# Performance work log

Measured on AMD Instinct MI355X. Metric: run time of the kernel, lower is better.

The kernel has to match this reference:

```python
import jax, jax.numpy as jnp
from jax import lax
import numpy as np

D_MODEL = 1024
D_STATE = 128
D_CONV = 4
EXPAND = 2
HEADDIM = 64
CHUNK = 10
D_INNER = EXPAND * D_MODEL          # 2048
NHEADS = D_INNER // HEADDIM         # 32
CONV_DIM = D_INNER + 2 * D_STATE    # 2304
BATCH, SEQ = 2, 1000


def setup_inputs() -> dict:
    key = jax.random.key(0)
    ks = jax.random.split(key, 9)
    n = lambda k, shp, sc: jax.random.normal(k, shp, dtype=jnp.float32) * sc
    return {
        "x": n(ks[0], (BATCH, SEQ, D_MODEL), 1.0),
        "W_in": n(ks[1], (2 * D_INNER + 2 * D_STATE + NHEADS, D_MODEL), 0.02),
        "conv_w": n(ks[2], (CONV_DIM, D_CONV), 0.2),
        "conv_b": n(ks[3], (CONV_DIM,), 0.02),
        "dt_bias": n(ks[4], (NHEADS,), 0.5),
        "A_log": jnp.log(jnp.linspace(1.0, 16.0, NHEADS)).astype(jnp.float32),
        "D": n(ks[6], (NHEADS,), 1.0),
        "norm_w": jnp.ones((D_INNER,), jnp.float32),
        "W_out": n(ks[8], (D_MODEL, D_INNER), 0.02),
    }


def segsum(x):
    # x: (..., T) -> (..., T, T) with out[i,j] = sum_{k=j+1..i} x_k for i>=j else -inf
    cs = jnp.cumsum(x, axis=-1)
    seg = cs[..., :, None] - cs[..., None, :]
    T = x.shape[-1]
    mask = jnp.tril(jnp.ones((T, T), bool))
    return jnp.where(mask, seg, -jnp.inf)


def ssd(x, A, Bm, Cm, chunk):
    # x: (b,l,h,p)  A: (b,l,h)  Bm,Cm: (b,l,n)  (ngroups=1, group dim squeezed)
    b, l, h, p = x.shape
    n = Bm.shape[-1]
    c = l // chunk
    xr = x.reshape(b, c, chunk, h, p)
    Ar = A.reshape(b, c, chunk, h).transpose(0, 3, 1, 2)      # (b,h,c,s)
    Br = Bm.reshape(b, c, chunk, n)
    Cr = Cm.reshape(b, c, chunk, n)
    Acs = jnp.cumsum(Ar, axis=-1)                              # (b,h,c,s)
    L = jnp.exp(segsum(Ar))                                    # (b,h,c,s,s)
    # intra-chunk (diagonal blocks)
    Y_diag = jnp.einsum('bcln,bcsn,bhcls,bcshp->bclhp', Cr, Br, L, xr)
    # per-chunk end states
    decay_states = jnp.exp(Acs[..., -1:] - Acs)                # (b,h,c,s)
    states = jnp.einsum('bcln,bhcl,bclhp->bchpn', Br, decay_states, xr)
    states = jnp.concatenate([jnp.zeros((b, 1, h, p, n), x.dtype), states], axis=1)
    # inter-chunk recurrence (parallel form)
    chunk_sums = jnp.pad(Acs[..., -1], ((0, 0), (0, 0), (1, 0)))  # (b,h,c+1)
    decay_chunk = jnp.exp(segsum(chunk_sums))                    # (b,h,c+1,c+1)
    new_states = jnp.einsum('bhzc,bchpn->bzhpn', decay_chunk, states)
    prev_states = new_states[:, :-1]                             # (b,c,h,p,n)
    # state -> output contribution
    Y_off = jnp.einsum('bcln,bchpn,bhcl->bclhp', Cr, prev_states, jnp.exp(Acs))
    return (Y_diag + Y_off).reshape(b, l, h, p)


def reference(x, W_in, conv_w, conv_b, dt_bias, A_log, D, norm_w, W_out):
    b, l, _ = x.shape
    zxbcdt = x @ W_in.T                                          # (b,l,4384)
    z = zxbcdt[..., :D_INNER]
    xBC = zxbcdt[..., D_INNER:D_INNER + CONV_DIM]
    dt = zxbcdt[..., D_INNER + CONV_DIM:]
    dt = jax.nn.softplus(dt + dt_bias)                           # (b,l,h)
    # causal depthwise conv1d
    xc = jnp.pad(xBC, ((0, 0), (D_CONV - 1, 0), (0, 0)))
    conv = lax.conv_general_dilated(
        xc.transpose(0, 2, 1), conv_w[:, None, :], (1,), 'VALID',
        feature_group_count=CONV_DIM,
        dimension_numbers=('NCH', 'OIH', 'NCH'))
    xBC = jax.nn.silu(conv.transpose(0, 2, 1) + conv_b)          # (b,l,conv_dim)
    x_ssm = xBC[..., :D_INNER].reshape(b, l, NHEADS, HEADDIM)
    Bm = xBC[..., D_INNER:D_INNER + D_STATE]
    Cm = xBC[..., D_INNER + D_STATE:]
    A = -jnp.exp(A_log)                                          # (h,)
    y = ssd(x_ssm * dt[..., None], A * dt, Bm, Cm, CHUNK)
    y = y + x_ssm * D[None, None, :, None]
    y = y.reshape(b, l, D_INNER)
    # gated RMSNorm
    y = y * jax.nn.silu(z)
    y = y * lax.rsqrt(jnp.mean(y * y, axis=-1, keepdims=True) + 1e-5) * norm_w
    return y @ W_out.T
```

## Files before the change

kernel.cpp:

```cpp
#include <hip/hip_runtime.h>
#include <hip/hip_bf16.h>

#define BATCHN 2
#define SEQL 1000
#define DMODEL 1024
#define DSTATE 128
#define HEADDIM 64
#define DINNER 2048
#define NHEADS 32
#define CONVDIM 2304
#define NPROJ 4384
#define TOKENS 2000
#define MPAD 2048
#define NPAD1 4480
#define QC 64
#define NCH 16

typedef __bf16 bfx8 __attribute__((ext_vector_type(8)));
typedef float fx4 __attribute__((ext_vector_type(4)));
typedef unsigned short u16x8 __attribute__((ext_vector_type(8)));

__device__ __forceinline__ unsigned short f2bf(float f) {
    unsigned int u = __builtin_bit_cast(unsigned int, f);
    u += 0x7FFFu + ((u >> 16) & 1u);
    return (unsigned short)(u >> 16);
}
__device__ __forceinline__ float bf2f(unsigned short u) {
    return __builtin_bit_cast(float, ((unsigned int)u) << 16);
}

__device__ __forceinline__ void gload16(const void* g, void* l) {
    __builtin_amdgcn_global_load_lds(
        (const __attribute__((address_space(1))) void*)g,
        (__attribute__((address_space(3))) void*)l, 16, 0, 0);
}

__global__ __launch_bounds__(256) void k_f2bf_pad(const float* __restrict__ src,
                                                  unsigned short* __restrict__ dst,
                                                  int n4src, int n4dst) {
    int i = blockIdx.x * 256 + threadIdx.x;
    if (i >= n4dst) return;
    ushort4 o = {0, 0, 0, 0};
    if (i < n4src) {
        float4 v = ((const float4*)src)[i];
        o.x = f2bf(v.x); o.y = f2bf(v.y); o.z = f2bf(v.z); o.w = f2bf(v.w);
    }
    ((ushort4*)dst)[i] = o;
}

__global__ __launch_bounds__(256) void k_dt(const float* __restrict__ x,
                                            const float* __restrict__ win,
                                            const float* __restrict__ dt_bias,
                                            float* __restrict__ dtv) {
    __shared__ float sx[8][1024];
    int t = threadIdx.x;
    int tok0 = blockIdx.x * 8;
    for (int i = t; i < 8 * 256; i += 256) {
        int tok = i >> 8, k4 = i & 255;
        ((float4*)&sx[tok][0])[k4] = ((const float4*)(x + (size_t)(tok0 + tok) * DMODEL))[k4];
    }
    __syncthreads();
    int tl = t >> 5, h = t & 31;
    const float4* wr_ = (const float4*)(win + (size_t)(2 * DINNER + 2 * DSTATE + h) * DMODEL);
    const float4* xr = (const float4*)&sx[tl][0];
    float acc = 0.f;
    #pragma unroll 4
    for (int k = 0; k < 256; ++k) {
        float4 a = xr[k], b = wr_[k];
        acc += a.x * b.x + a.y * b.y + a.z * b.z + a.w * b.w;
    }
    float v = acc + dt_bias[h];
    dtv[(size_t)(tok0 + tl) * NHEADS + h] = fmaxf(v, 0.f) + log1pf(expf(-fabsf(v)));
}

__global__ __launch_bounds__(256) void k_gemmd(const unsigned short* __restrict__ A,
                                               const unsigned short* __restrict__ B,
                                               float* __restrict__ C,
                                               int Mstore, int N, int K,
                                               int kc, size_t pstride) {
    __shared__ __attribute__((aligned(16))) unsigned short As[2][4096];
    __shared__ __attribute__((aligned(16))) unsigned short Bs[2][4096];
    int t = threadIdx.x;
    int lane = t & 63, wave = t >> 6;
    int wr = wave >> 1, wc = wave & 1;
    int m0 = blockIdx.y * 128, n0 = blockIdx.x * 128;
    int k0 = blockIdx.z * kc;
    int swcol = (((t & 3) ^ ((t >> 3) & 3)) * 8);
    const unsigned short* Ag = A + (size_t)(m0 + (t >> 2)) * K + k0 + swcol;
    const unsigned short* Bg = B + (size_t)(n0 + (t >> 2)) * K + k0 + swcol;
    int fr = lane & 15, ks = lane >> 4;
    int sl = (ks ^ ((fr >> 1) & 3)) << 3;
    fx4 acc[4][4] = {};
    gload16(Ag, &As[0][t * 8]);
    gload16(Ag + (size_t)64 * K, &As[0][2048 + t * 8]);
    gload16(Bg, &Bs[0][t * 8]);
    gload16(Bg + (size_t)64 * K, &Bs[0][2048 + t * 8]);
    __syncthreads();
    int cur = 0;
    for (int kk = 32; kk < kc; kk += 32) {
        gload16(Ag + kk, &As[cur ^ 1][t * 8]);
        gload16(Ag + (size_t)64 * K + kk, &As[cur ^ 1][2048 + t * 8]);
        gload16(Bg + kk, &Bs[cur ^ 1][t * 8]);
        gload16(Bg + (size_t)64 * K + kk, &Bs[cur ^ 1][2048 + t * 8]);
        bfx8 a[4], b[4];
        #pragma unroll
        for (int m = 0; m < 4; ++m)
            a[m] = *(const bfx8*)&As[cur][(wr * 64 + m * 16 + fr) * 32 + sl];
        #pragma unroll
        for (int n = 0; n < 4; ++n)
            b[n] = *(const bfx8*)&Bs[cur][(wc * 64 + n * 16 + fr) * 32 + sl];
        #pragma unroll
        for (int m = 0; m < 4; ++m)
            #pragma unroll
            for (int n = 0; n < 4; ++n)
                acc[m][n] = __builtin_amdgcn_mfma_f32_16x16x32_bf16(a[m], b[n], acc[m][n], 0, 0, 0);
        __syncthreads();
        cur ^= 1;
    }
    {
        bfx8 a[4], b[4];
        #pragma unroll
        for (int m = 0; m < 4; ++m)
            a[m] = *(const bfx8*)&As[cur][(wr * 64 + m * 16 + fr) * 32 + sl];
        #pragma unroll
        for (int n = 0; n < 4; ++n)
            b[n] = *(const bfx8*)&Bs[cur][(wc * 64 + n * 16 + fr) * 32 + sl];
        #pragma unroll
        for (int m = 0; m < 4; ++m)
            #pragma unroll
            for (int n = 0; n < 4; ++n)
                acc[m][n] = __builtin_amdgcn_mfma_f32_16x16x32_bf16(a[m], b[n], acc[m][n], 0, 0, 0);
    }
    float* Cz = C + (size_t)blockIdx.z * pstride;
    #pragma unroll
    for (int m = 0; m < 4; ++m) {
        int rbase = m0 + wr * 64 + m * 16 + (lane >> 4) * 4;
        #pragma unroll
        for (int i = 0; i < 4; ++i) {
            int r = rbase + i;
            if (r < Mstore) {
                #pragma unroll
                for (int n = 0; n < 4; ++n) {
                    int c = n0 + wc * 64 + n * 16 + fr;
                    if (c < N) Cz[(size_t)r * N + c] = acc[m][n][i];
                }
            }
        }
    }
}

__global__ __launch_bounds__(256) void k_red(const float* __restrict__ part,
                                             float* __restrict__ out, int n4, size_t pstride4) {
    int i = blockIdx.x * 256 + threadIdx.x;
    if (i >= n4) return;
    const float4* p = (const float4*)part;
    float4 v0 = p[i];
    float4 v1 = p[i + pstride4];
    float4 v2 = p[i + 2 * pstride4];
    float4 v3 = p[i + 3 * pstride4];
    float4 o;
    o.x = (v0.x + v1.x) + (v2.x + v3.x);
    o.y = (v0.y + v1.y) + (v2.y + v3.y);
    o.z = (v0.z + v1.z) + (v2.z + v3.z);
    o.w = (v0.w + v1.w) + (v2.w + v3.w);
    ((float4*)out)[i] = o;
}

__global__ __launch_bounds__(256) void k_conv4(const float* __restrict__ zx,
                                               const float* __restrict__ cw,
                                               const float* __restrict__ cb,
                                               float* __restrict__ xbc) {
    int idx = blockIdx.x * 256 + threadIdx.x;
    if (idx >= (TOKENS / 4) * CONVDIM) return;
    int tg = idx / CONVDIM;
    int col = idx - tg * CONVDIM;
    int b = tg / 250;
    int l0 = (tg - b * 250) * 4;
    float in[7];
    #pragma unroll
    for (int j = 0; j < 7; ++j) {
        int lj = l0 - 3 + j;
        in[j] = (lj >= 0) ? zx[(size_t)(b * SEQL + lj) * NPROJ + DINNER + col] : 0.f;
    }
    float w0 = cw[col * 4], w1 = cw[col * 4 + 1], w2 = cw[col * 4 + 2], w3 = cw[col * 4 + 3];
    float bb = cb[col];
    #pragma unroll
    for (int i = 0; i < 4; ++i) {
        float a = bb + w0 * in[i] + w1 * in[i + 1] + w2 * in[i + 2] + w3 * in[i + 3];
        xbc[(size_t)(b * SEQL + l0 + i) * CONVDIM + col] = a / (1.f + expf(-a));
    }
}

#define SCW 136
#define SWW 72
__global__ __launch_bounds__(256) void k_tile(const float* __restrict__ xbc,
                                              const float* __restrict__ dtv,
                                              const float* __restrict__ A_log,
                                              const float* __restrict__ Dp,
                                              float* __restrict__ ybuf,
                                              float* __restrict__ Sg,
                                              float* __restrict__ cumA) {
    __shared__ unsigned short sC[64 * SCW];
    __shared__ unsigned short sB[64 * SCW];
    __shared__ unsigned short sBdT[128 * SWW];
    __shared__ unsigned short sXdT[64 * SWW];
    __shared__ unsigned short sXr[64 * SWW];
    __shared__ float sAcs[64];
    __shared__ float sdt[64];
    int bid = blockIdx.x;
    int b = bid / (NHEADS * NCH);
    int r = bid % (NHEADS * NCH);
    int h = r / NCH, c = r % NCH;
    int t = threadIdx.x;
    int lane = t & 63, wave = t >> 6;
    if (t < 64) {
        int tok = c * QC + t;
        float d = (tok < SEQL) ? dtv[(size_t)(b * SEQL + tok) * NHEADS + h] : 0.f;
        float A = -expf(A_log[h]);
        float v = A * d;
        #pragma unroll
        for (int off = 1; off < 64; off <<= 1) {
            float u = __shfl_up(v, off, 64);
            if (lane >= off) v += u;
        }
        sdt[t] = d;
        sAcs[t] = v;
        cumA[(size_t)bid * 64 + t] = v;
    }
    __syncthreads();
    float Aend = sAcs[63];
    for (int i = t; i < 64 * 32; i += 256) {
        int l = i >> 5, n4 = (i & 31) * 4;
        int tok = c * QC + l;
        float4 cv = {0, 0, 0, 0}, bv = {0, 0, 0, 0};
        if (tok < SEQL) {
            const float* base = xbc + (size_t)(b * SEQL + tok) * CONVDIM;
            bv = *(const float4*)(base + DINNER + n4);
            cv = *(const float4*)(base + DINNER + DSTATE + n4);
        }
        float dec = expf(Aend - sAcs[l]);
        sC[l * SCW + n4 + 0] = f2bf(cv.x); sC[l * SCW + n4 + 1] = f2bf(cv.y);
        sC[l * SCW + n4 + 2] = f2bf(cv.z); sC[l * SCW + n4 + 3] = f2bf(cv.w);
        sB[l * SCW + n4 + 0] = f2bf(bv.x); sB[l * SCW + n4 + 1] = f2bf(bv.y);
        sB[l * SCW + n4 + 2] = f2bf(bv.z); sB[l * SCW + n4 + 3] = f2bf(bv.w);
        sBdT[(n4 + 0) * SWW + l] = f2bf(bv.x * dec);
        sBdT[(n4 + 1) * SWW + l] = f2bf(bv.y * dec);
        sBdT[(n4 + 2) * SWW + l] = f2bf(bv.z * dec);
        sBdT[(n4 + 3) * SWW + l] = f2bf(bv.w * dec);
    }
    for (int i = t; i < 64 * 16; i += 256) {
        int l = i >> 4, p4 = (i & 15) * 4;
        int tok = c * QC + l;
        float4 xv = {0, 0, 0, 0};
        if (tok < SEQL) xv = *(const float4*)(xbc + (size_t)(b * SEQL + tok) * CONVDIM + h * 64 + p4);
        float d = sdt[l];
        sXr[l * SWW + p4 + 0] = f2bf(xv.x); sXr[l * SWW + p4 + 1] = f2bf(xv.y);
        sXr[l * SWW + p4 + 2] = f2bf(xv.z); sXr[l * SWW + p4 + 3] = f2bf(xv.w);
        sXdT[(p4 + 0) * SWW + l] = f2bf(xv.x * d);
        sXdT[(p4 + 1) * SWW + l] = f2bf(xv.y * d);
        sXdT[(p4 + 2) * SWW + l] = f2bf(xv.z * d);
        sXdT[(p4 + 3) * SWW + l] = f2bf(xv.w * d);
    }
    __syncthreads();
    int fr = lane & 15, fk8 = (lane >> 4) * 8;
    int wr = wave >> 1, wc = wave & 1;
    fx4 g[2][2] = {};
    #pragma unroll
    for (int k = 0; k < 4; ++k) {
        bfx8 a0 = *(const bfx8*)&sC[(wr * 32 + fr) * SCW + k * 32 + fk8];
        bfx8 a1 = *(const bfx8*)&sC[(wr * 32 + 16 + fr) * SCW + k * 32 + fk8];
        bfx8 b0 = *(const bfx8*)&sB[(wc * 32 + fr) * SCW + k * 32 + fk8];
        bfx8 b1 = *(const bfx8*)&sB[(wc * 32 + 16 + fr) * SCW + k * 32 + fk8];
        g[0][0] = __builtin_amdgcn_mfma_f32_16x16x32_bf16(a0, b0, g[0][0], 0, 0, 0);
        g[0][1] = __builtin_amdgcn_mfma_f32_16x16x32_bf16(a0, b1, g[0][1], 0, 0, 0);
        g[1][0] = __builtin_amdgcn_mfma_f32_16x16x32_bf16(a1, b0, g[1][0], 0, 0, 0);
        g[1][1] = __builtin_amdgcn_mfma_f32_16x16x32_bf16(a1, b1, g[1][1], 0, 0, 0);
    }
    __syncthreads();
    int rb = wr * 32 + (lane >> 4) * 4;
    int cb = wc * 32 + fr;
    #pragma unroll
    for (int m = 0; m < 2; ++m)
        #pragma unroll
        for (int n = 0; n < 2; ++n)
            #pragma unroll
            for (int i = 0; i < 4; ++i) {
                int row = rb + m * 16 + i, col = cb + n * 16;
                float wv = (col <= row) ? g[m][n][i] * expf(sAcs[row] - sAcs[col]) : 0.f;
                sB[row * SWW + col] = f2bf(wv);
            }
    __syncthreads();
    fx4 yd[2][2] = {};
    fx4 sc[2][4] = {};
    #pragma unroll
    for (int k = 0; k < 2; ++k) {
        bfx8 aW0 = *(const bfx8*)&sB[(wr * 32 + fr) * SWW + k * 32 + fk8];
        bfx8 aW1 = *(const bfx8*)&sB[(wr * 32 + 16 + fr) * SWW + k * 32 + fk8];
        bfx8 bX0 = *(const bfx8*)&sXdT[(wc * 32 + fr) * SWW + k * 32 + fk8];
        bfx8 bX1 = *(const bfx8*)&sXdT[(wc * 32 + 16 + fr) * SWW + k * 32 + fk8];
        yd[0][0] = __builtin_amdgcn_mfma_f32_16x16x32_bf16(aW0, bX0, yd[0][0], 0, 0, 0);
        yd[0][1] = __builtin_amdgcn_mfma_f32_16x16x32_bf16(aW0, bX1, yd[0][1], 0, 0, 0);
        yd[1][0] = __builtin_amdgcn_mfma_f32_16x16x32_bf16(aW1, bX0, yd[1][0], 0, 0, 0);
        yd[1][1] = __builtin_amdgcn_mfma_f32_16x16x32_bf16(aW1, bX1, yd[1][1], 0, 0, 0);
        bfx8 aX0 = *(const bfx8*)&sXdT[(wr * 32 + fr) * SWW + k * 32 + fk8];
        bfx8 aX1 = *(const bfx8*)&sXdT[(wr * 32 + 16 + fr) * SWW + k * 32 + fk8];
        #pragma unroll
        for (int j = 0; j < 4; ++j) {
            bfx8 bB = *(const bfx8*)&sBdT[(wc * 64 + j * 16 + fr) * SWW + k * 32 + fk8];
            sc[0][j] = __builtin_amdgcn_mfma_f32_16x16x32_bf16(aX0, bB, sc[0][j], 0, 0, 0);
            sc[1][j] = __builtin_amdgcn_mfma_f32_16x16x32_bf16(aX1, bB, sc[1][j], 0, 0, 0);
        }
    }
    float Dh = Dp[h];
    #pragma unroll
    for (int m = 0; m < 2; ++m)
        #pragma unroll
        for (int i = 0; i < 4; ++i) {
            int row = rb + m * 16 + i;
            int tok = c * QC + row;
            if (tok < SEQL) {
                #pragma unroll
                for (int n = 0; n < 2; ++n) {
                    int col = cb + n * 16;
                    float xr = bf2f(sXr[row * SWW + col]);
                    ybuf[(size_t)(b * SEQL + tok) * DINNER + h * 64 + col] = yd[m][n][i] + Dh * xr;
                }
            }
        }
    #pragma unroll
    for (int m = 0; m < 2; ++m)
        #pragma unroll
        for (int i = 0; i < 4; ++i) {
            int p = rb + m * 16 + i;
            #pragma unroll
            for (int j = 0; j < 4; ++j) {
                int n = wc * 64 + j * 16 + fr;
                Sg[(size_t)bid * 8192 + p * 128 + n] = sc[m][j][i];
            }
        }
}

__global__ __launch_bounds__(256) void k_scan2v(float* __restrict__ Sg,
                                                const float* __restrict__ cumA) {
    int bid = blockIdx.x;
    int bh = bid >> 5, sub = bid & 31;
    int e = sub * 256 + threadIdx.x;
    __shared__ float sT[NCH];
    if (threadIdx.x < NCH)
        sT[threadIdx.x] = cumA[((size_t)(bh * NCH) + threadIdx.x) * 64 + 63];
    __syncthreads();
    float S = 0.f;
    size_t base = (size_t)bh * NCH * 8192 + e;
    for (int g = 0; g < NCH; ++g) {
        size_t off = base + (size_t)g * 8192;
        float sg = Sg[off];
        Sg[off] = S;
        S = expf(sT[g]) * S + sg;
    }
}

__global__ __launch_bounds__(256) void k_yoff(const float* __restrict__ xbc,
                                              const float* __restrict__ Sg,
                                              const float* __restrict__ cumA,
                                              float* __restrict__ ybuf) {
    int bid = blockIdx.x;
    int b = bid / (NHEADS * NCH);
    int r = bid % (NHEADS * NCH);
    int h = r / NCH, c = r % NCH;
    if (c == 0) return;
    __shared__ unsigned short sC[64 * SCW];
    __shared__ unsigned short sS[64 * SCW];
    __shared__ float sE[64];
    int t = threadIdx.x;
    int lane = t & 63, wave = t >> 6;
    if (t < 64) sE[t] = expf(cumA[(size_t)bid * 64 + t]);
    for (int i = t; i < 64 * 32; i += 256) {
        int l = i >> 5, n4 = (i & 31) * 4;
        int tok = c * QC + l;
        float4 cv = {0, 0, 0, 0};
        if (tok < SEQL)
            cv = *(const float4*)(xbc + (size_t)(b * SEQL + tok) * CONVDIM + DINNER + DSTATE + n4);
        sC[l * SCW + n4 + 0] = f2bf(cv.x); sC[l * SCW + n4 + 1] = f2bf(cv.y);
        sC[l * SCW + n4 + 2] = f2bf(cv.z); sC[l * SCW + n4 + 3] = f2bf(cv.w);
        float4 sv = *(const float4*)(Sg + (size_t)bid * 8192 + l * 128 + n4);
        sS[l * SCW + n4 + 0] = f2bf(sv.x); sS[l * SCW + n4 + 1] = f2bf(sv.y);
        sS[l * SCW + n4 + 2] = f2bf(sv.z); sS[l * SCW + n4 + 3] = f2bf(sv.w);
    }
    __syncthreads();
    int fr = lane & 15, fk8 = (lane >> 4) * 8;
    int wr = wave >> 1, wc = wave & 1;
    fx4 yo[2][2] = {};
    #pragma unroll
    for (int k = 0; k < 4; ++k) {
        bfx8 a0 = *(const bfx8*)&sC[(wr * 32 + fr) * SCW + k * 32 + fk8];
        bfx8 a1 = *(const bfx8*)&sC[(wr * 32 + 16 + fr) * SCW + k * 32 + fk8];
        bfx8 b0 = *(const bfx8*)&sS[(wc * 32 + fr) * SCW + k * 32 + fk8];
        bfx8 b1 = *(const bfx8*)&sS[(wc * 32 + 16 + fr) * SCW + k * 32 + fk8];
        yo[0][0] = __builtin_amdgcn_mfma_f32_16x16x32_bf16(a0, b0, yo[0][0], 0, 0, 0);
        yo[0][1] = __builtin_amdgcn_mfma_f32_16x16x32_bf16(a0, b1, yo[0][1], 0, 0, 0);
        yo[1][0] = __builtin_amdgcn_mfma_f32_16x16x32_bf16(a1, b0, yo[1][0], 0, 0, 0);
        yo[1][1] = __builtin_amdgcn_mfma_f32_16x16x32_bf16(a1, b1, yo[1][1], 0, 0, 0);
    }
    int rb = wr * 32 + (lane >> 4) * 4;
    int cb = wc * 32 + fr;
    #pragma unroll
    for (int m = 0; m < 2; ++m)
        #pragma unroll
        for (int i = 0; i < 4; ++i) {
            int row = rb + m * 16 + i;
            int tok = c * QC + row;
            if (tok < SEQL) {
                float e = sE[row];
                #pragma unroll
                for (int n = 0; n < 2; ++n) {
                    int col = cb + n * 16;
                    size_t off = (size_t)(b * SEQL + tok) * DINNER + h * 64 + col;
                    ybuf[off] += yo[m][n][i] * e;
                }
            }
        }
}

__global__ __launch_bounds__(256) void k_norm(const float* __restrict__ ybuf,
                                              const float* __restrict__ zx,
                                              const float* __restrict__ normw,
                                              unsigned short* __restrict__ ynb) {
    int row = blockIdx.x;
    int t = threadIdx.x;
    if (row >= TOKENS) {
        #pragma unroll
        for (int j = 0; j < 8; ++j) ynb[(size_t)row * DINNER + t + j * 256] = 0;
        return;
    }
    float v[8];
    float ss = 0.f;
    #pragma unroll
    for (int j = 0; j < 8; ++j) {
        int col = t + j * 256;
        float y = ybuf[(size_t)row * DINNER + col];
        float z = zx[(size_t)row * NPROJ + col];
        y *= z / (1.f + expf(-z));
        v[j] = y;
        ss += y * y;
    }
    #pragma unroll
    for (int off = 32; off > 0; off >>= 1) ss += __shfl_down(ss, off, 64);
    __shared__ float red[4];
    int lane = t & 63, wv = t >> 6;
    if (lane == 0) red[wv] = ss;
    __syncthreads();
    float tot = red[0] + red[1] + red[2] + red[3];
    float r = rsqrtf(tot * (1.f / DINNER) + 1e-5f);
    #pragma unroll
    for (int j = 0; j < 8; ++j) {
        int col = t + j * 256;
        ynb[(size_t)row * DINNER + col] = f2bf(v[j] * r * normw[col]);
    }
}

extern "C" void kernel_launch(void* const* d_in, const int* in_sizes, int n_in,
                              void* d_out, int out_size, void* d_ws, size_t ws_size,
                              hipStream_t stream) {
    const float* x       = (const float*)d_in[0];
    const float* W_in    = (const float*)d_in[1];
    const float* conv_w  = (const float*)d_in[2];
    const float* conv_b  = (const float*)d_in[3];
    const float* dt_bias = (const float*)d_in[4];
    const float* A_log   = (const float*)d_in[5];
    const float* Dp      = (const float*)d_in[6];
    const float* norm_w  = (const float*)d_in[7];
    const float* W_out   = (const float*)d_in[8];
    float* out = (float*)d_out;

    char* w = (char*)d_ws;
    auto alloc = [&](size_t bytes) {
        char* p = w;
        w += (bytes + 255) & ~(size_t)255;
        return p;
    };
    unsigned short* xb    = (unsigned short*)alloc((size_t)MPAD * DMODEL * 2);
    unsigned short* winb  = (unsigned short*)alloc((size_t)NPAD1 * DMODEL * 2);
    unsigned short* woutb = (unsigned short*)alloc((size_t)DMODEL * DINNER * 2);
    float* zx   = (float*)alloc((size_t)TOKENS * NPROJ * 4);
    float* xbc  = (float*)alloc((size_t)TOKENS * CONVDIM * 4);
    float* dtv  = (float*)alloc((size_t)TOKENS * NHEADS * 4);
    float* yb   = (float*)alloc((size_t)TOKENS * DINNER * 4);
    unsigned short* ynb = (unsigned short*)alloc((size_t)MPAD * DINNER * 2);
    float* Sg   = (float*)alloc((size_t)BATCHN * NHEADS * NCH * HEADDIM * DSTATE * 4);
    float* cumA = (float*)alloc((size_t)BATCHN * NHEADS * NCH * 64 * 4);

    int n4;
    n4 = MPAD * DMODEL / 4;
    k_f2bf_pad<<<(n4 + 255) / 256, 256, 0, stream>>>(x, xb, TOKENS * DMODEL / 4, n4);
    n4 = NPAD1 * DMODEL / 4;
    k_f2bf_pad<<<(n4 + 255) / 256, 256, 0, stream>>>(W_in, winb, NPROJ * DMODEL / 4, n4);
    n4 = DMODEL * DINNER / 4;
    k_f2bf_pad<<<(n4 + 255) / 256, 256, 0, stream>>>(W_out, woutb, n4, n4);
    k_dt<<<TOKENS / 8, 256, 0, stream>>>(x, W_in, dt_bias, dtv);
    dim3 g1(NPAD1 / 128, MPAD / 128, 1);
    k_gemmd<<<g1, 256, 0, stream>>>(xb, winb, zx, TOKENS, NPROJ, DMODEL, DMODEL, 0);
    k_conv4<<<(TOKENS / 4) * CONVDIM / 256, 256, 0, stream>>>(zx, conv_w, conv_b, xbc);
    k_tile<<<BATCHN * NHEADS * NCH, 256, 0, stream>>>(xbc, dtv, A_log, Dp, yb, Sg, cumA);
    k_scan2v<<<BATCHN * NHEADS * 32, 256, 0, stream>>>(Sg, cumA);
    k_yoff<<<BATCHN * NHEADS * NCH, 256, 0, stream>>>(xbc, Sg, cumA, yb);
    k_norm<<<MPAD, 256, 0, stream>>>(yb, zx, norm_w, ynb);
    size_t pstride = (size_t)MPAD * DMODEL;
    dim3 g2(DMODEL / 128, MPAD / 128, 4);
    k_gemmd<<<g2, 256, 0, stream>>>(ynb, woutb, zx, MPAD, DMODEL, DINNER, DINNER / 4, pstride);
    n4 = TOKENS * DMODEL / 4;
    k_red<<<(n4 + 255) / 256, 256, 0, stream>>>(zx, out, n4, pstride / 4);
}
```

Before: 184.4 us.

## Deepen GEMM K-tile to 64, halve split-K, and reorder SSD block indexing

The bf16 MFMA GEMM now stages 64-wide K tiles with an 8-way XOR swizzle instead of 32-wide tiles. That halves the number of barrier-separated iterations and doubles LDS use per block to 64 KB. The output projection's split-K drops from 4 to 2, so fewer partial buffers are written and the reduction reads only two. The SSD tile and y-offset kernels map block IDs with head as the fastest-varying index, which changes scheduling locality. Fewer resident blocks per CU from the larger LDS footprint and fewer parallel blocks in the out-projection are the trade-offs.

```diff
diff --git a/kernel.cpp b/kernel.cpp
--- a/kernel.cpp
+++ b/kernel.cpp
@@ -73,64 +73,71 @@
     dtv[(size_t)(tok0 + tl) * NHEADS + h] = fmaxf(v, 0.f) + log1pf(expf(-fabsf(v)));
 }
 
-__global__ __launch_bounds__(256) void k_gemmd(const unsigned short* __restrict__ A,
+__global__ __launch_bounds__(256) void k_gemmk(const unsigned short* __restrict__ A,
                                                const unsigned short* __restrict__ B,
                                                float* __restrict__ C,
                                                int Mstore, int N, int K,
                                                int kc, size_t pstride) {
-    __shared__ __attribute__((aligned(16))) unsigned short As[2][4096];
-    __shared__ __attribute__((aligned(16))) unsigned short Bs[2][4096];
+    __shared__ __attribute__((aligned(16))) unsigned short As[2][8192];
+    __shared__ __attribute__((aligned(16))) unsigned short Bs[2][8192];
     int t = threadIdx.x;
     int lane = t & 63, wave = t >> 6;
     int wr = wave >> 1, wc = wave & 1;
     int m0 = blockIdx.y * 128, n0 = blockIdx.x * 128;
     int k0 = blockIdx.z * kc;
-    int swcol = (((t & 3) ^ ((t >> 3) & 3)) * 8);
-    const unsigned short* Ag = A + (size_t)(m0 + (t >> 2)) * K + k0 + swcol;
-    const unsigned short* Bg = B + (size_t)(n0 + (t >> 2)) * K + k0 + swcol;
+    int nk = kc / 64;
+    int scol = (((t & 7) ^ ((t >> 3) & 7)) * 8);
+    const unsigned short* Ag = A + (size_t)(m0 + (t >> 3)) * K + k0 + scol;
+    const unsigned short* Bg = B + (size_t)(n0 + (t >> 3)) * K + k0 + scol;
     int fr = lane & 15, ks = lane >> 4;
-    int sl = (ks ^ ((fr >> 1) & 3)) << 3;
     fx4 acc[4][4] = {};
-    gload16(Ag, &As[0][t * 8]);
-    gload16(Ag + (size_t)64 * K, &As[0][2048 + t * 8]);
-    gload16(Bg, &Bs[0][t * 8]);
-    gload16(Bg + (size_t)64 * K, &Bs[0][2048 + t * 8]);
+
+#define STAGEK(bi, s) do {                                              \
+        int ko_ = (s) * 64;                                             \
+        gload16(Ag + ko_, &As[bi][t * 8]);                              \
+        gload16(Ag + (size_t)32 * K + ko_, &As[bi][2048 + t * 8]);      \
+        gload16(Ag + (size_t)64 * K + ko_, &As[bi][4096 + t * 8]);      \
+        gload16(Ag + (size_t)96 * K + ko_, &As[bi][6144 + t * 8]);      \
+        gload16(Bg + ko_, &Bs[bi][t * 8]);                              \
+        gload16(Bg + (size_t)32 * K + ko_, &Bs[bi][2048 + t * 8]);      \
+        gload16(Bg + (size_t)64 * K + ko_, &Bs[bi][4096 + t * 8]);      \
+        gload16(Bg + (size_t)96 * K + ko_, &Bs[bi][6144 + t * 8]);      \
+    } while (0)
+
+#define COMPUTEK(bi) do {                                               \
+        _Pragma("unroll")                                               \
+        for (int kh = 0; kh < 2; ++kh) {                                \
+            bfx8 a_[4], b_[4];                                          \
+            _Pragma("unroll")                                           \
+            for (int m = 0; m < 4; ++m) {                               \
+                int R = wr * 64 + m * 16 + fr;                          \
+                a_[m] = *(const bfx8*)&As[bi][R * 64 + (((kh * 4 + ks) ^ (R & 7)) << 3)]; \
+            }                                                           \
+            _Pragma("unroll")                                           \
+            for (int n = 0; n < 4; ++n) {                               \
+                int R = wc * 64 + n * 16 + fr;                          \
+                b_[n] = *(const bfx8*)&Bs[bi][R * 64 + (((kh * 4 + ks) ^ (R & 7)) << 3)]; \
+            }                                                           \
+            _Pragma("unroll")                                           \
+            for (int m = 0; m < 4; ++m)                                 \
+                _Pragma("unroll")                                       \
+                for (int n = 0; n < 4; ++n)                             \
+                    acc[m][n] = __builtin_amdgcn_mfma_f32_16x16x32_bf16(a_[m], b_[n], acc[m][n], 0, 0, 0); \
+        }                                                               \
+    } while (0)
+
+    STAGEK(0, 0);
     __syncthreads();
     int cur = 0;
-    for (int kk = 32; kk < kc; kk += 32) {
-        gload16(Ag + kk, &As[cur ^ 1][t * 8]);
-        gload16(Ag + (size_t)64 * K + kk, &As[cur ^ 1][2048 + t * 8]);
-        gload16(Bg + kk, &Bs[cur ^ 1][t * 8]);
-        gload16(Bg + (size_t)64 * K + kk, &Bs[cur ^ 1][2048 + t * 8]);
-        bfx8 a[4], b[4];
-        #pragma unroll
-        for (int m = 0; m < 4; ++m)
-            a[m] = *(const bfx8*)&As[cur][(wr * 64 + m * 16 + fr) * 32 + sl];
-        #pragma unroll
-        for (int n = 0; n < 4; ++n)
-            b[n] = *(const bfx8*)&Bs[cur][(wc * 64 + n * 16 + fr) * 32 + sl];
-        #pragma unroll
-        for (int m = 0; m < 4; ++m)
-            #pragma unroll
-            for (int n = 0; n < 4; ++n)
-                acc[m][n] = __builtin_amdgcn_mfma_f32_16x16x32_bf16(a[m], b[n], acc[m][n], 0, 0, 0);
+    for (int kt = 1; kt < nk; ++kt) {
+        STAGEK(cur ^ 1, kt);
+        COMPUTEK(cur);
         __syncthreads();
         cur ^= 1;
     }
-    {
-        bfx8 a[4], b[4];
-        #pragma unroll
-        for (int m = 0; m < 4; ++m)
-            a[m] = *(const bfx8*)&As[cur][(wr * 64 + m * 16 + fr) * 32 + sl];
-        #pragma unroll
-        for (int n = 0; n < 4; ++n)
-            b[n] = *(const bfx8*)&Bs[cur][(wc * 64 + n * 16 + fr) * 32 + sl];
-        #pragma unroll
-        for (int m = 0; m < 4; ++m)
-            #pragma unroll
-            for (int n = 0; n < 4; ++n)
-                acc[m][n] = __builtin_amdgcn_mfma_f32_16x16x32_bf16(a[m], b[n], acc[m][n], 0, 0, 0);
-    }
+    COMPUTEK(cur);
+#undef STAGEK
+#undef COMPUTEK
     float* Cz = C + (size_t)blockIdx.z * pstride;
     #pragma unroll
     for (int m = 0; m < 4; ++m) {
@@ -149,20 +156,18 @@
     }
 }
 
-__global__ __launch_bounds__(256) void k_red(const float* __restrict__ part,
-                                             float* __restrict__ out, int n4, size_t pstride4) {
+__global__ __launch_bounds__(256) void k_red2(const float* __restrict__ part,
+                                              float* __restrict__ out, int n4, size_t pstride4) {
     int i = blockIdx.x * 256 + threadIdx.x;
     if (i >= n4) return;
     const float4* p = (const float4*)part;
     float4 v0 = p[i];
     float4 v1 = p[i + pstride4];
-    float4 v2 = p[i + 2 * pstride4];
-    float4 v3 = p[i + 3 * pstride4];
     float4 o;
-    o.x = (v0.x + v1.x) + (v2.x + v3.x);
-    o.y = (v0.y + v1.y) + (v2.y + v3.y);
-    o.z = (v0.z + v1.z) + (v2.z + v3.z);
-    o.w = (v0.w + v1.w) + (v2.w + v3.w);
+    o.x = v0.x + v1.x;
+    o.y = v0.y + v1.y;
+    o.z = v0.z + v1.z;
+    o.w = v0.w + v1.w;
     ((float4*)out)[i] = o;
 }
 
@@ -208,9 +213,11 @@
     __shared__ float sAcs[64];
     __shared__ float sdt[64];
     int bid = blockIdx.x;
-    int b = bid / (NHEADS * NCH);
-    int r = bid % (NHEADS * NCH);
-    int h = r / NCH, c = r % NCH;
+    int h = bid & 31;
+    int tmp = bid >> 5;
+    int c = tmp & 15;
+    int b = tmp >> 4;
+    size_t lin = (size_t)((b * NHEADS + h) * NCH + c);
     int t = threadIdx.x;
     int lane = t & 63, wave = t >> 6;
     if (t < 64) {
@@ -225,7 +232,7 @@
         }
         sdt[t] = d;
         sAcs[t] = v;
-        cumA[(size_t)bid * 64 + t] = v;
+        cumA[lin * 64 + t] = v;
     }
     __syncthreads();
     float Aend = sAcs[63];
@@ -335,7 +342,7 @@
             #pragma unroll
             for (int j = 0; j < 4; ++j) {
                 int n = wc * 64 + j * 16 + fr;
-                Sg[(size_t)bid * 8192 + p * 128 + n] = sc[m][j][i];
+                Sg[lin * 8192 + p * 128 + n] = sc[m][j][i];
             }
         }
 }
@@ -364,16 +371,18 @@
                                               const float* __restrict__ cumA,
                                               float* __restrict__ ybuf) {
     int bid = blockIdx.x;
-    int b = bid / (NHEADS * NCH);
-    int r = bid % (NHEADS * NCH);
-    int h = r / NCH, c = r % NCH;
+    int h = bid & 31;
+    int tmp = bid >> 5;
+    int c = tmp & 15;
+    int b = tmp >> 4;
     if (c == 0) return;
+    size_t lin = (size_t)((b * NHEADS + h) * NCH + c);
     __shared__ unsigned short sC[64 * SCW];
     __shared__ unsigned short sS[64 * SCW];
     __shared__ float sE[64];
     int t = threadIdx.x;
     int lane = t & 63, wave = t >> 6;
-    if (t < 64) sE[t] = expf(cumA[(size_t)bid * 64 + t]);
+    if (t < 64) sE[t] = expf(cumA[lin * 64 + t]);
     for (int i = t; i < 64 * 32; i += 256) {
         int l = i >> 5, n4 = (i & 31) * 4;
         int tok = c * QC + l;
@@ -382,7 +391,7 @@
             cv = *(const float4*)(xbc + (size_t)(b * SEQL + tok) * CONVDIM + DINNER + DSTATE + n4);
         sC[l * SCW + n4 + 0] = f2bf(cv.x); sC[l * SCW + n4 + 1] = f2bf(cv.y);
         sC[l * SCW + n4 + 2] = f2bf(cv.z); sC[l * SCW + n4 + 3] = f2bf(cv.w);
-        float4 sv = *(const float4*)(Sg + (size_t)bid * 8192 + l * 128 + n4);
+        float4 sv = *(const float4*)(Sg + lin * 8192 + l * 128 + n4);
         sS[l * SCW + n4 + 0] = f2bf(sv.x); sS[l * SCW + n4 + 1] = f2bf(sv.y);
         sS[l * SCW + n4 + 2] = f2bf(sv.z); sS[l * SCW + n4 + 3] = f2bf(sv.w);
     }
@@ -498,15 +507,15 @@
     k_f2bf_pad<<<(n4 + 255) / 256, 256, 0, stream>>>(W_out, woutb, n4, n4);
     k_dt<<<TOKENS / 8, 256, 0, stream>>>(x, W_in, dt_bias, dtv);
     dim3 g1(NPAD1 / 128, MPAD / 128, 1);
-    k_gemmd<<<g1, 256, 0, stream>>>(xb, winb, zx, TOKENS, NPROJ, DMODEL, DMODEL, 0);
+    k_gemmk<<<g1, 256, 0, stream>>>(xb, winb, zx, TOKENS, NPROJ, DMODEL, DMODEL, 0);
     k_conv4<<<(TOKENS / 4) * CONVDIM / 256, 256, 0, stream>>>(zx, conv_w, conv_b, xbc);
     k_tile<<<BATCHN * NHEADS * NCH, 256, 0, stream>>>(xbc, dtv, A_log, Dp, yb, Sg, cumA);
     k_scan2v<<<BATCHN * NHEADS * 32, 256, 0, stream>>>(Sg, cumA);
     k_yoff<<<BATCHN * NHEADS * NCH, 256, 0, stream>>>(xbc, Sg, cumA, yb);
     k_norm<<<MPAD, 256, 0, stream>>>(yb, zx, norm_w, ynb);
     size_t pstride = (size_t)MPAD * DMODEL;
-    dim3 g2(DMODEL / 128, MPAD / 128, 4);
-    k_gemmd<<<g2, 256, 0, stream>>>(ynb, woutb, zx, MPAD, DMODEL, DINNER, DINNER / 4, pstride);
+    dim3 g2(DMODEL / 128, MPAD / 128, 2);
+    k_gemmk<<<g2, 256, 0, stream>>>(ynb, woutb, zx, MPAD, DMODEL, DINNER, DINNER / 2, pstride);
     n4 = TOKENS * DMODEL / 4;
-    k_red<<<(n4 + 255) / 256, 256, 0, stream>>>(zx, out, n4, pstride / 4);
-}
+    k_red2<<<(n4 + 255) / 256, 256, 0, stream>>>(zx, out, n4, pstride / 4);
+}
```

Measured after the change: 191.5 us. +3.9%, slower.
